# Optimization experiments

Measured on AMD Instinct MI355X. Metric: run time of the kernel, lower is better.

The kernel has to match this reference:

```python
import jax, jax.numpy as jnp
import numpy as np

D_MODEL = 768
N_HEADS = 12
D_HEAD = 64
WINDOW = 32
LOOK_BACK = 1
PAD_VALUE = 0
IGNORE = -1000000.0
BS = 2
SEQ = 1024  # multiple of WINDOW so autopad is a no-op


def setup_inputs() -> dict:
    key = jax.random.key(0)
    k0, k1, k2, k3, k4 = jax.random.split(key, 5)
    x = jax.random.normal(k0, (BS, SEQ, D_MODEL), dtype=jnp.float32)
    W_abcde = jax.random.normal(k1, (D_MODEL, 5 * N_HEADS * D_HEAD), dtype=jnp.float32) * (1.0 / np.sqrt(D_MODEL))
    b_abcde = jax.random.normal(k2, (5 * N_HEADS * D_HEAD,), dtype=jnp.float32) * 0.02
    W_O = jax.random.normal(k3, (N_HEADS * D_HEAD, D_MODEL), dtype=jnp.float32) * (1.0 / np.sqrt(N_HEADS * D_HEAD))
    b_O = jax.random.normal(k4, (D_MODEL,), dtype=jnp.float32) * 0.02
    return dict(x=x, W_abcde=W_abcde, b_abcde=b_abcde, W_O=W_O, b_O=b_O)


def _look_around(t, backward=LOOK_BACK, pad_value=0):
    # t: (B, n_windows, window, ...). Pad along the windows axis, then
    # concatenate [prev_window, current_window] along the within-window axis.
    nw = t.shape[1]
    pad = [(0, 0)] * t.ndim
    pad[1] = (backward, 0)
    tp = jnp.pad(t, pad, constant_values=pad_value)
    return jnp.concatenate([tp[:, i:i + nw] for i in range(backward + 1)], axis=2)


def reference(x, W_abcde, b_abcde, W_O, b_O):
    bs, ts, _ = x.shape
    nw = ts // WINDOW
    B = bs * N_HEADS

    abcde = x @ W_abcde + b_abcde                       # (bs, ts, 5*h*d)
    abcde = abcde.reshape(bs, ts, 5, N_HEADS, D_HEAD)
    abcde = jnp.transpose(abcde, (2, 0, 3, 1, 4))       # (5, bs, h, ts, d)
    abcde = abcde.reshape(5, B, nw, WINDOW, D_HEAD)     # windowed
    a, b, c, d, e = abcde[0], abcde[1], abcde[2], abcde[3], abcde[4]

    # position ids per window, and their look-around version (pad_value = cfg.pad_value)
    seq = jnp.arange(ts, dtype=jnp.int32).reshape(1, nw, WINDOW)      # (1, nw, w)
    bb_t = _look_around(seq, LOOK_BACK, PAD_VALUE)                    # (1, nw, 2w)
    qi = seq[..., :, None, None]    # query position  (n axis)
    kj = bb_t[..., None, :, None]   # a-token position (m axis)
    lk = bb_t[..., None, None, :]   # b-token position (l axis)
    # masked unless: t_b <= t_query AND t_a < t_b
    mask = (qi < lk) | (lk <= kj)   # (1, nw, w, 2w, 2w)

    la_a = _look_around(a)
    la_b = _look_around(b)
    la_d = _look_around(d)
    la_e = _look_around(e)

    # triple-interaction scores: (B, nw, w, 2w, 2w)
    attn = jnp.einsum('xnid,xnjd,xnkd->xnijk', c, la_a, la_b)
    # mask causal-invalid entries, and (as in original) exact zeros (padding dots)
    attn = jnp.where(mask | (attn == 0.0), IGNORE, attn)
    attn = attn / D_HEAD
    shp = attn.shape
    score = jax.nn.softmax(attn.reshape(shp[0], shp[1], shp[2], -1), axis=-1).reshape(shp)

    # dual value combine: D at the a-position (m), E at the b-position (l)
    z = jnp.einsum('xnijk,xnjd->xnid', score, la_d) \
        + jnp.einsum('xnijk,xnkd->xnid', score, la_e)

    z = z.reshape(bs, N_HEADS, nw, WINDOW, D_HEAD)
    z = jnp.transpose(z, (0, 2, 3, 1, 4)).reshape(bs, ts, N_HEADS * D_HEAD)
    return z @ W_O + b_O
```

## Files before the change

### kernel.cpp

```cpp
#include <hip/hip_runtime.h>
#include <math.h>
#include <stdint.h>

#define NH     12
#define DH     64
#define WIN    32
#define SEQL   1024
#define BSZ    2
#define NW     (SEQL / WIN)
#define DMODEL 768
#define NCOL   (5 * NH * DH)

typedef __attribute__((ext_vector_type(4))) float f32x4;
typedef __attribute__((ext_vector_type(8))) short bf16x8;
typedef unsigned short u16;

static __device__ __forceinline__ u16 f2bf(float f) {
  union { float f; unsigned u; } v; v.f = f;
  unsigned r = v.u + 0x7fffu + ((v.u >> 16) & 1u);
  return (u16)(r >> 16);
}
static __device__ __forceinline__ float bf2f(u16 u) {
  union { unsigned u; float f; } v; v.u = ((unsigned)u) << 16;
  return v.f;
}

typedef const __attribute__((address_space(1))) unsigned int* as1_cu32;
typedef __attribute__((address_space(3))) unsigned int* as3_u32;
static __device__ __forceinline__ void gload_lds16(const void* g, void* l) {
  __builtin_amdgcn_global_load_lds(
      reinterpret_cast<as1_cu32>(reinterpret_cast<uintptr_t>(g)),
      reinterpret_cast<as3_u32>(reinterpret_cast<uintptr_t>(l)), 16, 0, 0);
}

__global__ __launch_bounds__(256)
void cvt_bf16_kernel(const float* __restrict__ S, u16* __restrict__ D, int n4) {
  const int i = blockIdx.x * 256 + threadIdx.x;
  if (i < n4) {
    const float4 v = reinterpret_cast<const float4*>(S)[i];
    ushort4 o;
    o.x = f2bf(v.x); o.y = f2bf(v.y); o.z = f2bf(v.z); o.w = f2bf(v.w);
    reinterpret_cast<ushort4*>(D)[i] = o;
  }
}

__global__ __launch_bounds__(256)
void transpose_cvt_kernel(const float* __restrict__ S, u16* __restrict__ D,
                          int K, int N) {
  __shared__ u16 tile[64][68];
  const int tid = threadIdx.x;
  const int n0 = blockIdx.x * 64;
  const int k0 = blockIdx.y * 64;
#pragma unroll
  for (int pass = 0; pass < 4; ++pass) {
    const int r = pass * 16 + (tid >> 4);
    const int c = (tid & 15) << 2;
    const float4 v = *reinterpret_cast<const float4*>(&S[(size_t)(k0 + r) * N + n0 + c]);
    tile[c + 0][r] = f2bf(v.x); tile[c + 1][r] = f2bf(v.y);
    tile[c + 2][r] = f2bf(v.z); tile[c + 3][r] = f2bf(v.w);
  }
  __syncthreads();
#pragma unroll
  for (int pass = 0; pass < 4; ++pass) {
    const int rn = pass * 16 + (tid >> 4);
    const int ck = (tid & 15) << 2;
    ushort4 o;
    o.x = tile[rn][ck + 0]; o.y = tile[rn][ck + 1];
    o.z = tile[rn][ck + 2]; o.w = tile[rn][ck + 3];
    *reinterpret_cast<ushort4*>(&D[(size_t)(n0 + rn) * K + k0 + ck]) = o;
  }
}

template<int BM, int BN, int WAVES_M, int WAVES_N, bool OUT_BF16>
__global__ __launch_bounds__(256)
void gemm_mfma_kernel(const u16* __restrict__ A, const u16* __restrict__ Bt,
                      const float* __restrict__ bias, void* __restrict__ Cout,
                      int M, int N, int K) {
  constexpr int BK = 64;
  constexpr int MT = BM / (16 * WAVES_M);
  constexpr int NT = BN / (16 * WAVES_N);
  constexpr int CHA = BM / 8;
  constexpr int CHB = BN / 8;
  __shared__ __align__(16) u16 As[BM * BK];
  __shared__ __align__(16) u16 Bs[BN * BK];

  const int tid  = threadIdx.x;
  const int w    = tid >> 6;
  const int lane = tid & 63;
  const int m16  = lane & 15;
  const int g    = lane >> 4;
  const int wr   = w / WAVES_N;
  const int wc   = w % WAVES_N;
  const int bm   = blockIdx.y * BM;
  const int bn   = blockIdx.x * BN;

  const int srow   = lane >> 3;
  const int srcCol = ((lane & 7) ^ srow) << 3;

  f32x4 acc[MT][NT];
#pragma unroll
  for (int i = 0; i < MT; ++i)
#pragma unroll
    for (int j = 0; j < NT; ++j) {
      f32x4 z = {0.f, 0.f, 0.f, 0.f};
      acc[i][j] = z;
    }

  for (int k0 = 0; k0 < K; k0 += BK) {
#pragma unroll
    for (int c = 0; c < CHA / 4; ++c) {
      const int ch = w * (CHA / 4) + c;
      const int r  = ch * 8 + srow;
      gload_lds16(A + (size_t)(bm + r) * K + k0 + srcCol, As + ch * 512);
    }
#pragma unroll
    for (int c = 0; c < CHB / 4; ++c) {
      const int ch = w * (CHB / 4) + c;
      const int r  = ch * 8 + srow;
      gload_lds16(Bt + (size_t)(bn + r) * K + k0 + srcCol, Bs + ch * 512);
    }
    __syncthreads();

#pragma unroll
    for (int kk = 0; kk < 2; ++kk) {
      const int cs = (((kk << 2) + g) ^ (m16 & 7)) << 3;
      bf16x8 af[MT], bf[NT];
#pragma unroll
      for (int i = 0; i < MT; ++i) {
        const int r = wr * (16 * MT) + i * 16 + m16;
        af[i] = *reinterpret_cast<const bf16x8*>(&As[r * 64 + cs]);
      }
#pragma unroll
      for (int j = 0; j < NT; ++j) {
        const int r = wc * (16 * NT) + j * 16 + m16;
        bf[j] = *reinterpret_cast<const bf16x8*>(&Bs[r * 64 + cs]);
      }
#pragma unroll
      for (int i = 0; i < MT; ++i)
#pragma unroll
        for (int j = 0; j < NT; ++j)
          acc[i][j] = __builtin_amdgcn_mfma_f32_16x16x32_bf16(af[i], bf[j], acc[i][j], 0, 0, 0);
    }
    __syncthreads();
  }

#pragma unroll
  for (int i = 0; i < MT; ++i) {
#pragma unroll
    for (int j = 0; j < NT; ++j) {
      const int col = bn + wc * 16 * NT + j * 16 + m16;
      const float bcol = bias[col];
#pragma unroll
      for (int rr = 0; rr < 4; ++rr) {
        const int row = bm + wr * 16 * MT + i * 16 + g * 4 + rr;
        const float v = acc[i][j][rr] + bcol;
        if (OUT_BF16)
          reinterpret_cast<u16*>(Cout)[(size_t)row * N + col] = f2bf(v);
        else
          reinterpret_cast<float*>(Cout)[(size_t)row * N + col] = v;
      }
    }
  }
}

__global__ __launch_bounds__(256, 2)
void attn_mfma_kernel(const u16* __restrict__ Y, u16* __restrict__ Z) {
  __shared__ __align__(16) u16 DET[64][136];
  __shared__ __align__(16) u16 RQ[32][136];
  __shared__ float tot_lds[32];

  const int n  = blockIdx.x;
  const int bh = blockIdx.y;
  const int bi = bh / NH;
  const int h  = bh % NH;
  const int tid  = threadIdx.x;
  const int wv   = tid >> 6;
  const int lane = tid & 63;
  const int m16  = lane & 15;
  const int g    = lane >> 4;
  const u16* Yb = Y + (size_t)bi * SEQL * NCOL;

  {
    const int j = tid >> 2;
    const int q = tid & 3;
    const int t = n * WIN - WIN + j;
    if (t >= 0) {
      const u16* dr = Yb + (size_t)t * NCOL + (3 * NH + h) * DH + q * 16;
      const u16* er = Yb + (size_t)t * NCOL + (4 * NH + h) * DH + q * 16;
      const bf16x8 d0 = *reinterpret_cast<const bf16x8*>(dr);
      const bf16x8 d1 = *reinterpret_cast<const bf16x8*>(dr + 8);
      const bf16x8 e0 = *reinterpret_cast<const bf16x8*>(er);
      const bf16x8 e1 = *reinterpret_cast<const bf16x8*>(er + 8);
#pragma unroll
      for (int e = 0; e < 8; ++e) {
        DET[q * 16 + e][j]          = (u16)d0[e];
        DET[q * 16 + 8 + e][j]      = (u16)d1[e];
        DET[q * 16 + e][64 + j]     = (u16)e0[e];
        DET[q * 16 + 8 + e][64 + j] = (u16)e1[e];
      }
    } else {
#pragma unroll
      for (int e = 0; e < 16; ++e) {
        DET[q * 16 + e][j] = 0;
        DET[q * 16 + e][64 + j] = 0;
      }
    }
  }

  bf16x8 afr[4][2];
#pragma unroll
  for (int jt = 0; jt < 4; ++jt) {
    const int j = jt * 16 + m16;
    const int t = n * WIN - WIN + j;
#pragma unroll
    for (int ks = 0; ks < 2; ++ks) {
      if (n == 0 && jt < 2) {
        bf16x8 z = {0, 0, 0, 0, 0, 0, 0, 0};
        afr[jt][ks] = z;
      } else {
        afr[jt][ks] = *reinterpret_cast<const bf16x8*>(
            Yb + (size_t)t * NCOL + h * DH + ks * 32 + g * 8);
      }
    }
  }
  float bfr[4][2][8];
#pragma unroll
  for (int kt = 0; kt < 4; ++kt) {
    const int k = kt * 16 + m16;
    const int t = n * WIN - WIN + k;
#pragma unroll
    for (int ks = 0; ks < 2; ++ks) {
      if (n == 0 && kt < 2) {
#pragma unroll
        for (int e = 0; e < 8; ++e) bfr[kt][ks][e] = 0.f;
      } else {
        const bf16x8 braw = *reinterpret_cast<const bf16x8*>(
            Yb + (size_t)t * NCOL + (NH + h) * DH + ks * 32 + g * 8);
#pragma unroll
        for (int e = 0; e < 8; ++e) bfr[kt][ks][e] = bf2f((u16)braw[e]);
      }
    }
  }

  const float NEG_INF = -__builtin_inff();
  const u16* crow_base = Yb + (size_t)(n * WIN) * NCOL + (2 * NH + h) * DH;

  for (int ii = 0; ii < 8; ++ii) {
    const int i = wv * 8 + ii;
    const u16* cp = crow_base + (size_t)i * NCOL;

    float cf[2][8];
#pragma unroll
    for (int ks = 0; ks < 2; ++ks) {
      const bf16x8 craw = *reinterpret_cast<const bf16x8*>(cp + ks * 32 + g * 8);
#pragma unroll
      for (int e = 0; e < 8; ++e) cf[ks][e] = bf2f((u16)craw[e]);
    }

    f32x4 acc[4][4];
#pragma unroll
    for (int jt = 0; jt < 4; ++jt)
#pragma unroll
      for (int kt = 0; kt < 4; ++kt) {
        f32x4 z = {0.f, 0.f, 0.f, 0.f};
        acc[jt][kt] = z;
      }

#pragma unroll
    for (int ks = 0; ks < 2; ++ks) {
#pragma unroll
      for (int kt = 0; kt < 4; ++kt) {
        bf16x8 vf;
#pragma unroll
        for (int e = 0; e < 8; ++e) vf[e] = (short)f2bf(bfr[kt][ks][e] * cf[ks][e]);
#pragma unroll
        for (int jt = 0; jt < 4; ++jt)
          acc[jt][kt] = __builtin_amdgcn_mfma_f32_16x16x32_bf16(afr[jt][ks], vf, acc[jt][kt], 0, 0, 0);
      }
    }

    float m = NEG_INF;
#pragma unroll
    for (int jt = 0; jt < 4; ++jt)
#pragma unroll
      for (int kt = 0; kt < 4; ++kt)
#pragma unroll
        for (int r = 0; r < 4; ++r) {
          const int j = jt * 16 + g * 4 + r;
          const int k = kt * 16 + m16;
          const bool valid = (k > j) && (k <= i + 32) && (n > 0 || j >= 32);
          const float s = valid ? acc[jt][kt][r] : NEG_INF;
          acc[jt][kt][r] = s;
          m = fmaxf(m, s);
        }
#pragma unroll
    for (int off = 32; off >= 1; off >>= 1) m = fmaxf(m, __shfl_xor(m, off));

    const bool degen = (n == 0 && i == 0);
    float rsel, qsel, tp;
    if (!degen) {
      float rpf[16];
      float qp[4];
#pragma unroll
      for (int u = 0; u < 16; ++u) rpf[u] = 0.f;
#pragma unroll
      for (int u = 0; u < 4; ++u) qp[u] = 0.f;
#pragma unroll
      for (int jt = 0; jt < 4; ++jt)
#pragma unroll
        for (int kt = 0; kt < 4; ++kt)
#pragma unroll
          for (int r = 0; r < 4; ++r) {
            const float e = __expf((acc[jt][kt][r] - m) * 0.015625f);
            rpf[jt * 4 + r] += e;
            qp[kt] += e;
          }
#pragma unroll
      for (int u = 0; u < 16; ++u) {
        float v = rpf[u];
        v += __shfl_xor(v, 1); v += __shfl_xor(v, 2);
        v += __shfl_xor(v, 4); v += __shfl_xor(v, 8);
        rpf[u] = v;
      }
#pragma unroll
      for (int u = 0; u < 4; ++u) {
        float v = qp[u];
        v += __shfl_xor(v, 16); v += __shfl_xor(v, 32);
        qp[u] = v;
      }
      float t = 0.f;
#pragma unroll
      for (int u = 0; u < 16; ++u) t += rpf[u];
      t += __shfl_xor(t, 16); t += __shfl_xor(t, 32);
      tp = t;
      float f8[8];
#pragma unroll
      for (int u = 0; u < 8; ++u) f8[u] = (m16 & 1) ? rpf[2 * u + 1] : rpf[2 * u];
      float f4s[4];
#pragma unroll
      for (int u = 0; u < 4; ++u) f4s[u] = (m16 & 2) ? f8[2 * u + 1] : f8[2 * u];
      float f2s[2];
#pragma unroll
      for (int u = 0; u < 2; ++u) f2s[u] = (m16 & 4) ? f4s[2 * u + 1] : f4s[2 * u];
      rsel = (m16 & 8) ? f2s[1] : f2s[0];
      const float q2a = (g & 1) ? qp[1] : qp[0];
      const float q2b = (g & 1) ? qp[3] : qp[2];
      qsel = (g & 2) ? q2b : q2a;
    } else {
      rsel = 1.f; qsel = 1.f; tp = 64.f;
    }

    RQ[i][(m16 >> 2) * 16 + g * 4 + (m16 & 3)] = f2bf(rsel);
    RQ[i][64 + g * 16 + m16] = f2bf(qsel);
    if (lane == 0) tot_lds[i] = tp;
  }

  __syncthreads();

  const int nt = wv;
  f32x4 zac[2];
  {
    f32x4 z = {0.f, 0.f, 0.f, 0.f};
    zac[0] = z; zac[1] = z;
  }
#pragma unroll
  for (int kq = 0; kq < 4; ++kq) {
    const bf16x8 bf = *reinterpret_cast<const bf16x8*>(&DET[nt * 16 + m16][kq * 32 + g * 8]);
#pragma unroll
    for (int mt = 0; mt < 2; ++mt) {
      const bf16x8 af = *reinterpret_cast<const bf16x8*>(&RQ[mt * 16 + m16][kq * 32 + g * 8]);
      zac[mt] = __builtin_amdgcn_mfma_f32_16x16x32_bf16(af, bf, zac[mt], 0, 0, 0);
    }
  }
#pragma unroll
  for (int mt = 0; mt < 2; ++mt)
#pragma unroll
    for (int r = 0; r < 4; ++r) {
      const int i = mt * 16 + g * 4 + r;
      const int d = nt * 16 + m16;
      const float inv = 1.0f / tot_lds[i];
      Z[((size_t)bi * SEQL + n * WIN + i) * (NH * DH) + h * DH + d] =
          f2bf(zac[mt][r] * inv);
    }
}

extern "C" void kernel_launch(void* const* d_in, const int* in_sizes, int n_in,
                              void* d_out, int out_size, void* d_ws, size_t ws_size,
                              hipStream_t stream) {
  const float* x        = (const float*)d_in[0];
  const float* W_abcde  = (const float*)d_in[1];
  const float* b_abcde  = (const float*)d_in[2];
  const float* W_O      = (const float*)d_in[3];
  const float* b_O      = (const float*)d_in[4];
  float* out = (float*)d_out;

  const int M = BSZ * SEQL;

  u16* Yb  = (u16*)d_ws;
  u16* xb  = Yb  + (size_t)M * NCOL;
  u16* Wt  = xb  + (size_t)M * DMODEL;
  u16* WOt = Wt  + (size_t)NCOL * DMODEL;
  u16* Zb  = WOt + (size_t)(NH * DH) * DMODEL;

  cvt_bf16_kernel<<<(M * DMODEL / 4 + 255) / 256, 256, 0, stream>>>(x, xb, M * DMODEL / 4);
  transpose_cvt_kernel<<<dim3(NCOL / 64, DMODEL / 64), 256, 0, stream>>>(W_abcde, Wt, DMODEL, NCOL);
  transpose_cvt_kernel<<<dim3((NH * DH) / 64, DMODEL / 64), 256, 0, stream>>>(W_O, WOt, DMODEL, NH * DH);

  gemm_mfma_kernel<128, 128, 2, 2, true><<<dim3(NCOL / 128, M / 128), 256, 0, stream>>>(
      xb, Wt, b_abcde, Yb, M, NCOL, DMODEL);

  attn_mfma_kernel<<<dim3(NW, BSZ * NH), 256, 0, stream>>>(Yb, Zb);

  gemm_mfma_kernel<64, 64, 2, 2, false><<<dim3((NH * DH) / 64, M / 64), 256, 0, stream>>>(
      Zb, WOt, b_O, out, M, DMODEL, NH * DH);
}
```

Baseline: 174.6 us.

## Use 512-thread attention blocks, drop softmax max pass, shuffle-reduce rows

Doubles the attention block to 8 waves so each wave handles 4 query rows instead of 8, and splits the final Z MFMA across waves by row tile. It removes the max-subtraction pass and computes unnormalized exp2 directly, relying on scores being small enough not to overflow. It keeps the b operand as packed bf16 to cut register use, and replaces the select-tree reductions with butterfly shuffle-add transposes. The risks are exp overflow without max subtraction and register pressure under the 512-thread launch bound.

```diff
diff --git a/kernel.cpp b/kernel.cpp
--- a/kernel.cpp
+++ b/kernel.cpp
@@ -163,7 +163,7 @@
   }
 }
 
-__global__ __launch_bounds__(256, 2)
+__global__ __launch_bounds__(512, 3)
 void attn_mfma_kernel(const u16* __restrict__ Y, u16* __restrict__ Z) {
   __shared__ __align__(16) u16 DET[64][136];
   __shared__ __align__(16) u16 RQ[32][136];
@@ -181,81 +181,62 @@
   const u16* Yb = Y + (size_t)bi * SEQL * NCOL;
 
   {
-    const int j = tid >> 2;
-    const int q = tid & 3;
-    const int t = n * WIN - WIN + j;
+    const int j  = lane;
+    const int r8 = wv * 8;
+    const int t  = n * WIN - WIN + j;
     if (t >= 0) {
-      const u16* dr = Yb + (size_t)t * NCOL + (3 * NH + h) * DH + q * 16;
-      const u16* er = Yb + (size_t)t * NCOL + (4 * NH + h) * DH + q * 16;
-      const bf16x8 d0 = *reinterpret_cast<const bf16x8*>(dr);
-      const bf16x8 d1 = *reinterpret_cast<const bf16x8*>(dr + 8);
-      const bf16x8 e0 = *reinterpret_cast<const bf16x8*>(er);
-      const bf16x8 e1 = *reinterpret_cast<const bf16x8*>(er + 8);
+      const bf16x8 dv = *reinterpret_cast<const bf16x8*>(
+          Yb + (size_t)t * NCOL + (3 * NH + h) * DH + r8);
+      const bf16x8 ev = *reinterpret_cast<const bf16x8*>(
+          Yb + (size_t)t * NCOL + (4 * NH + h) * DH + r8);
 #pragma unroll
       for (int e = 0; e < 8; ++e) {
-        DET[q * 16 + e][j]          = (u16)d0[e];
-        DET[q * 16 + 8 + e][j]      = (u16)d1[e];
-        DET[q * 16 + e][64 + j]     = (u16)e0[e];
-        DET[q * 16 + 8 + e][64 + j] = (u16)e1[e];
+        DET[r8 + e][j]      = (u16)dv[e];
+        DET[r8 + e][64 + j] = (u16)ev[e];
       }
     } else {
 #pragma unroll
-      for (int e = 0; e < 16; ++e) {
-        DET[q * 16 + e][j] = 0;
-        DET[q * 16 + e][64 + j] = 0;
-      }
-    }
-  }
-
-  bf16x8 afr[4][2];
+      for (int e = 0; e < 8; ++e) {
+        DET[r8 + e][j] = 0;
+        DET[r8 + e][64 + j] = 0;
+      }
+    }
+  }
+
+  bf16x8 afr[4][2], bfrb[4][2];
 #pragma unroll
   for (int jt = 0; jt < 4; ++jt) {
-    const int j = jt * 16 + m16;
-    const int t = n * WIN - WIN + j;
+    const int t = n * WIN - WIN + jt * 16 + m16;
 #pragma unroll
     for (int ks = 0; ks < 2; ++ks) {
       if (n == 0 && jt < 2) {
         bf16x8 z = {0, 0, 0, 0, 0, 0, 0, 0};
         afr[jt][ks] = z;
+        bfrb[jt][ks] = z;
       } else {
         afr[jt][ks] = *reinterpret_cast<const bf16x8*>(
             Yb + (size_t)t * NCOL + h * DH + ks * 32 + g * 8);
-      }
-    }
-  }
-  float bfr[4][2][8];
-#pragma unroll
-  for (int kt = 0; kt < 4; ++kt) {
-    const int k = kt * 16 + m16;
-    const int t = n * WIN - WIN + k;
-#pragma unroll
-    for (int ks = 0; ks < 2; ++ks) {
-      if (n == 0 && kt < 2) {
-#pragma unroll
-        for (int e = 0; e < 8; ++e) bfr[kt][ks][e] = 0.f;
-      } else {
-        const bf16x8 braw = *reinterpret_cast<const bf16x8*>(
+        bfrb[jt][ks] = *reinterpret_cast<const bf16x8*>(
             Yb + (size_t)t * NCOL + (NH + h) * DH + ks * 32 + g * 8);
-#pragma unroll
-        for (int e = 0; e < 8; ++e) bfr[kt][ks][e] = bf2f((u16)braw[e]);
-      }
-    }
-  }
-
-  const float NEG_INF = -__builtin_inff();
+      }
+    }
+  }
+
+  const float K2 = 0.015625f * 1.44269504088896341f;
   const u16* crow_base = Yb + (size_t)(n * WIN) * NCOL + (2 * NH + h) * DH;
 
-  for (int ii = 0; ii < 8; ++ii) {
-    const int i = wv * 8 + ii;
+  for (int ii = 0; ii < 4; ++ii) {
+    const int i = wv * 4 + ii;
     const u16* cp = crow_base + (size_t)i * NCOL;
 
+    bf16x8 craw[2];
+    craw[0] = *reinterpret_cast<const bf16x8*>(cp + g * 8);
+    craw[1] = *reinterpret_cast<const bf16x8*>(cp + 32 + g * 8);
     float cf[2][8];
 #pragma unroll
-    for (int ks = 0; ks < 2; ++ks) {
-      const bf16x8 craw = *reinterpret_cast<const bf16x8*>(cp + ks * 32 + g * 8);
-#pragma unroll
-      for (int e = 0; e < 8; ++e) cf[ks][e] = bf2f((u16)craw[e]);
-    }
+    for (int ks = 0; ks < 2; ++ks)
+#pragma unroll
+      for (int e = 0; e < 8; ++e) cf[ks][e] = bf2f((u16)craw[ks][e]);
 
     f32x4 acc[4][4];
 #pragma unroll
@@ -272,82 +253,98 @@
       for (int kt = 0; kt < 4; ++kt) {
         bf16x8 vf;
 #pragma unroll
-        for (int e = 0; e < 8; ++e) vf[e] = (short)f2bf(bfr[kt][ks][e] * cf[ks][e]);
+        for (int e = 0; e < 8; ++e)
+          vf[e] = (short)f2bf(bf2f((u16)bfrb[kt][ks][e]) * cf[ks][e]);
 #pragma unroll
         for (int jt = 0; jt < 4; ++jt)
           acc[jt][kt] = __builtin_amdgcn_mfma_f32_16x16x32_bf16(afr[jt][ks], vf, acc[jt][kt], 0, 0, 0);
       }
     }
 
-    float m = NEG_INF;
-#pragma unroll
-    for (int jt = 0; jt < 4; ++jt)
-#pragma unroll
-      for (int kt = 0; kt < 4; ++kt)
+    float rp[16], qp[4];
+#pragma unroll
+    for (int u = 0; u < 16; ++u) rp[u] = 0.f;
+#pragma unroll
+    for (int u = 0; u < 4; ++u) qp[u] = 0.f;
+#pragma unroll
+    for (int kt = 0; kt < 4; ++kt) {
+      const int k = kt * 16 + m16;
+      const bool ck = k <= i + 32;
+#pragma unroll
+      for (int jt = 0; jt < 4; ++jt) {
+        const bool rok = (n > 0) || (jt >= 2);
 #pragma unroll
         for (int r = 0; r < 4; ++r) {
           const int j = jt * 16 + g * 4 + r;
-          const int k = kt * 16 + m16;
-          const bool valid = (k > j) && (k <= i + 32) && (n > 0 || j >= 32);
-          const float s = valid ? acc[jt][kt][r] : NEG_INF;
-          acc[jt][kt][r] = s;
-          m = fmaxf(m, s);
+          const bool valid = ck && rok && (k > j);
+          const float e = valid ? exp2f(acc[jt][kt][r] * K2) : 0.f;
+          rp[jt * 4 + r] += e;
+          qp[kt] += e;
         }
-#pragma unroll
-    for (int off = 32; off >= 1; off >>= 1) m = fmaxf(m, __shfl_xor(m, off));
-
-    const bool degen = (n == 0 && i == 0);
+      }
+    }
+
     float rsel, qsel, tp;
-    if (!degen) {
-      float rpf[16];
-      float qp[4];
-#pragma unroll
-      for (int u = 0; u < 16; ++u) rpf[u] = 0.f;
-#pragma unroll
-      for (int u = 0; u < 4; ++u) qp[u] = 0.f;
-#pragma unroll
-      for (int jt = 0; jt < 4; ++jt)
-#pragma unroll
-        for (int kt = 0; kt < 4; ++kt)
-#pragma unroll
-          for (int r = 0; r < 4; ++r) {
-            const float e = __expf((acc[jt][kt][r] - m) * 0.015625f);
-            rpf[jt * 4 + r] += e;
-            qp[kt] += e;
-          }
-#pragma unroll
-      for (int u = 0; u < 16; ++u) {
-        float v = rpf[u];
-        v += __shfl_xor(v, 1); v += __shfl_xor(v, 2);
-        v += __shfl_xor(v, 4); v += __shfl_xor(v, 8);
-        rpf[u] = v;
-      }
-#pragma unroll
-      for (int u = 0; u < 4; ++u) {
-        float v = qp[u];
-        v += __shfl_xor(v, 16); v += __shfl_xor(v, 32);
-        qp[u] = v;
-      }
-      float t = 0.f;
-#pragma unroll
-      for (int u = 0; u < 16; ++u) t += rpf[u];
-      t += __shfl_xor(t, 16); t += __shfl_xor(t, 32);
-      tp = t;
-      float f8[8];
-#pragma unroll
-      for (int u = 0; u < 8; ++u) f8[u] = (m16 & 1) ? rpf[2 * u + 1] : rpf[2 * u];
-      float f4s[4];
-#pragma unroll
-      for (int u = 0; u < 4; ++u) f4s[u] = (m16 & 2) ? f8[2 * u + 1] : f8[2 * u];
-      float f2s[2];
-#pragma unroll
-      for (int u = 0; u < 2; ++u) f2s[u] = (m16 & 4) ? f4s[2 * u + 1] : f4s[2 * u];
-      rsel = (m16 & 8) ? f2s[1] : f2s[0];
-      const float q2a = (g & 1) ? qp[1] : qp[0];
-      const float q2b = (g & 1) ? qp[3] : qp[2];
-      qsel = (g & 2) ? q2b : q2a;
+    if (n == 0 && i == 0) {
+      rsel = 1.f; qsel = 1.f; tp = 64.f;
     } else {
-      rsel = 1.f; qsel = 1.f; tp = 64.f;
+      float tin = (qp[0] + qp[1]) + (qp[2] + qp[3]);
+#pragma unroll
+      for (int off = 1; off <= 32; off <<= 1) tin += __shfl_xor(tin, off);
+      tp = tin;
+
+      float v8[8];
+      {
+        const bool b = (m16 & 1) != 0;
+#pragma unroll
+        for (int t2 = 0; t2 < 8; ++t2) {
+          const float keep = b ? rp[2 * t2 + 1] : rp[2 * t2];
+          const float send = b ? rp[2 * t2] : rp[2 * t2 + 1];
+          v8[t2] = keep + __shfl_xor(send, 1);
+        }
+      }
+      float v4s[4];
+      {
+        const bool b = (m16 & 2) != 0;
+#pragma unroll
+        for (int t2 = 0; t2 < 4; ++t2) {
+          const float keep = b ? v8[2 * t2 + 1] : v8[2 * t2];
+          const float send = b ? v8[2 * t2] : v8[2 * t2 + 1];
+          v4s[t2] = keep + __shfl_xor(send, 2);
+        }
+      }
+      float v2s[2];
+      {
+        const bool b = (m16 & 4) != 0;
+#pragma unroll
+        for (int t2 = 0; t2 < 2; ++t2) {
+          const float keep = b ? v4s[2 * t2 + 1] : v4s[2 * t2];
+          const float send = b ? v4s[2 * t2] : v4s[2 * t2 + 1];
+          v2s[t2] = keep + __shfl_xor(send, 4);
+        }
+      }
+      {
+        const bool b = (m16 & 8) != 0;
+        const float keep = b ? v2s[1] : v2s[0];
+        const float send = b ? v2s[0] : v2s[1];
+        rsel = keep + __shfl_xor(send, 8);
+      }
+      float q2[2];
+      {
+        const bool b = (g & 1) != 0;
+#pragma unroll
+        for (int t2 = 0; t2 < 2; ++t2) {
+          const float keep = b ? qp[2 * t2 + 1] : qp[2 * t2];
+          const float send = b ? qp[2 * t2] : qp[2 * t2 + 1];
+          q2[t2] = keep + __shfl_xor(send, 16);
+        }
+      }
+      {
+        const bool b = (g & 2) != 0;
+        const float keep = b ? q2[1] : q2[0];
+        const float send = b ? q2[0] : q2[1];
+        qsel = keep + __shfl_xor(send, 32);
+      }
     }
 
     RQ[i][(m16 >> 2) * 16 + g * 4 + (m16 & 3)] = f2bf(rsel);
@@ -357,31 +354,22 @@
 
   __syncthreads();
 
-  const int nt = wv;
-  f32x4 zac[2];
-  {
-    f32x4 z = {0.f, 0.f, 0.f, 0.f};
-    zac[0] = z; zac[1] = z;
-  }
+  const int mt = wv >> 2;
+  const int nt = wv & 3;
+  f32x4 zac = {0.f, 0.f, 0.f, 0.f};
 #pragma unroll
   for (int kq = 0; kq < 4; ++kq) {
     const bf16x8 bf = *reinterpret_cast<const bf16x8*>(&DET[nt * 16 + m16][kq * 32 + g * 8]);
-#pragma unroll
-    for (int mt = 0; mt < 2; ++mt) {
-      const bf16x8 af = *reinterpret_cast<const bf16x8*>(&RQ[mt * 16 + m16][kq * 32 + g * 8]);
-      zac[mt] = __builtin_amdgcn_mfma_f32_16x16x32_bf16(af, bf, zac[mt], 0, 0, 0);
-    }
-  }
-#pragma unroll
-  for (int mt = 0; mt < 2; ++mt)
-#pragma unroll
-    for (int r = 0; r < 4; ++r) {
-      const int i = mt * 16 + g * 4 + r;
-      const int d = nt * 16 + m16;
-      const float inv = 1.0f / tot_lds[i];
-      Z[((size_t)bi * SEQL + n * WIN + i) * (NH * DH) + h * DH + d] =
-          f2bf(zac[mt][r] * inv);
-    }
+    const bf16x8 af = *reinterpret_cast<const bf16x8*>(&RQ[mt * 16 + m16][kq * 32 + g * 8]);
+    zac = __builtin_amdgcn_mfma_f32_16x16x32_bf16(af, bf, zac, 0, 0, 0);
+  }
+#pragma unroll
+  for (int r = 0; r < 4; ++r) {
+    const int i = mt * 16 + g * 4 + r;
+    const int d = nt * 16 + m16;
+    Z[((size_t)bi * SEQL + n * WIN + i) * (NH * DH) + h * DH + d] =
+        f2bf(zac[r] / tot_lds[i]);
+  }
 }
 
 extern "C" void kernel_launch(void* const* d_in, const int* in_sizes, int n_in,
@@ -409,7 +397,7 @@
   gemm_mfma_kernel<128, 128, 2, 2, true><<<dim3(NCOL / 128, M / 128), 256, 0, stream>>>(
       xb, Wt, b_abcde, Yb, M, NCOL, DMODEL);
 
-  attn_mfma_kernel<<<dim3(NW, BSZ * NH), 256, 0, stream>>>(Yb, Zb);
+  attn_mfma_kernel<<<dim3(NW, BSZ * NH), 512, 0, stream>>>(Yb, Zb);
 
   gemm_mfma_kernel<64, 64, 2, 2, false><<<dim3((NH * DH) / 64, M / 64), 256, 0, stream>>>(
       Zb, WOt, b_O, out, M, DMODEL, NH * DH);
```

Result: faster. 161.7 us (-7.4%).
